# Optimization experiments

Measured on AMD Instinct MI355X. Metric: run time of the kernel, lower is better.

Reference implementation:

```python
import jax, jax.numpy as jnp
import numpy as np

N = 50000      # nodes
E = 800000     # edges (avg degree 16)
F_IN = 128     # input features
HID = 64       # hidden per head
HEADS = 4      # heads per layer
G = 256        # graphs in batch
C = 10         # classes
ALPHA = 0.01   # leaky relu negative slope


def setup_inputs() -> dict:
    key = jax.random.key(0)
    ks = jax.random.split(key, 12)
    x = jax.random.normal(ks[0], (N, F_IN), dtype=jnp.float32)
    edge_index = jax.random.randint(ks[1], (2, E), 0, N, dtype=jnp.int32)
    batch = jnp.sort(jax.random.randint(ks[2], (N,), 0, G, dtype=jnp.int32))

    def glorot(k, shape):
        fan_in = shape[0] if len(shape) == 2 else int(np.prod(shape[1:]))
        return (jax.random.normal(k, shape, dtype=jnp.float32) / np.float32(np.sqrt(fan_in)))

    W1 = glorot(ks[3], (F_IN, HEADS * HID))
    a1_src = glorot(ks[4], (HEADS, HID))
    a1_dst = glorot(ks[5], (HEADS, HID))
    W2 = glorot(ks[6], (HEADS * HID, HEADS * HID))
    a2_src = glorot(ks[7], (HEADS, HID))
    a2_dst = glorot(ks[8], (HEADS, HID))
    lin_W = glorot(ks[9], (2 * HEADS * HID, C))
    lin_b = jnp.zeros((C,), dtype=jnp.float32)
    return {
        "x": x, "edge_index": edge_index, "batch": batch,
        "W1": W1, "a1_src": a1_src, "a1_dst": a1_dst,
        "W2": W2, "a2_src": a2_src, "a2_dst": a2_dst,
        "lin_W": lin_W, "lin_b": lin_b,
    }


def _gat_layer(x, src, dst, W, a_src, a_dst):
    """Multi-head GAT layer: edge softmax over incoming neighbors, concat heads, ELU."""
    n = x.shape[0]
    h, f = a_src.shape
    Wh = (x @ W).reshape(n, h, f)                       # [N,H,F]
    # per-node attention logits (decomposed GAT attention a^T [Wh_i || Wh_j])
    ls = jnp.einsum("nhf,hf->nh", Wh, a_src)            # [N,H]
    ld = jnp.einsum("nhf,hf->nh", Wh, a_dst)            # [N,H]
    e = jax.nn.leaky_relu(ls[src] + ld[dst], ALPHA)      # [E,H]
    # numerically-stable softmax over edges grouped by destination node
    m = jax.ops.segment_max(e, dst, num_segments=n)      # [N,H]
    m = jnp.where(jnp.isfinite(m), m, 0.0)
    p = jnp.exp(e - m[dst])                              # [E,H]
    z = jax.ops.segment_sum(p, dst, num_segments=n)      # [N,H]
    attn = p / (z[dst] + 1e-16)                          # [E,H]
    msg = Wh[src] * attn[:, :, None]                     # [E,H,F]
    out = jax.ops.segment_sum(msg, dst, num_segments=n)  # [N,H,F]
    return jax.nn.elu(out.reshape(n, h * f))


def reference(x, edge_index, batch, W1, a1_src, a1_dst, W2, a2_src, a2_dst, lin_W, lin_b):
    src, dst = edge_index[0], edge_index[1]
    x = _gat_layer(x, src, dst, W1, a1_src, a1_dst)
    x = _gat_layer(x, src, dst, W2, a2_src, a2_dst)
    # global max / mean pool per graph
    mx = jax.ops.segment_max(x, batch, num_segments=G)
    mx = jnp.where(jnp.isfinite(mx), mx, 0.0)
    s = jax.ops.segment_sum(x, batch, num_segments=G)
    cnt = jax.ops.segment_sum(jnp.ones((x.shape[0], 1), x.dtype), batch, num_segments=G)
    mean = s / jnp.maximum(cnt, 1.0)
    pooled = jnp.concatenate([mx, mean], axis=1)         # [G, 2*H*F]
    return pooled @ lin_W + lin_b                        # [G, C]
```

## Files before the change

kernel.cpp:

```cpp
#include <hip/hip_runtime.h>
#include <hip/hip_bf16.h>

#define NNODES 50000
#define NEDGES 800000
#define FIN    128
#define HID    64
#define HEADS  4
#define NGRAPH 256
#define NCLS   10
#define DTOT   256
#define ALPHA  0.01f
#define CAPLG  6
#define CAP    (1 << CAPLG)

typedef short bf16x8 __attribute__((ext_vector_type(8)));
typedef float f32x4  __attribute__((ext_vector_type(4)));

#define NB      ((NNODES + 255) / 256)
#define EB      ((NEDGES + 255) / 256)
#define XB      ((NNODES * FIN / 4 + 255) / 256)
#define W1B     (FIN * DTOT / 256)
#define W2B     (DTOT * DTOT / 256)

__device__ __forceinline__ ushort f2bf(float v) {
    return __bfloat16_as_ushort(__float2bfloat16(v));
}
__device__ __forceinline__ float blo(unsigned u) { return __uint_as_float(u << 16); }
__device__ __forceinline__ float bhi(unsigned u) { return __uint_as_float(u & 0xffff0000u); }

__global__ __launch_bounds__(256) void k_setup(const int* __restrict__ src, const int* __restrict__ dst,
                                               int* __restrict__ cursor, int* __restrict__ esrc,
                                               const int* __restrict__ batch, int* __restrict__ gstart,
                                               const float4* __restrict__ x4, ushort4* __restrict__ xbf4,
                                               const float* __restrict__ W1, ushort* __restrict__ W1t,
                                               const float* __restrict__ W2, ushort* __restrict__ W2t) {
    int b = blockIdx.x, t = threadIdx.x;
    if (b < EB) {
        int e = b * 256 + t;
        if (e < NEDGES) {
            int d = dst[e];
            int pos = atomicAdd(&cursor[d], 1);
            if (pos < CAP) esrc[(d << CAPLG) + pos] = src[e];
        }
    } else if (b < EB + NB) {
        int i = (b - EB) * 256 + t;
        if (i >= NNODES) return;
        int bb = batch[i];
        if (i == 0) {
            for (int g = 0; g <= bb; ++g) gstart[g] = 0;
        } else {
            int pb = batch[i - 1];
            if (pb != bb) for (int g = pb + 1; g <= bb; ++g) gstart[g] = i;
        }
        if (i == NNODES - 1)
            for (int g = bb + 1; g <= NGRAPH; ++g) gstart[g] = NNODES;
    } else if (b < EB + NB + XB) {
        int i = (b - EB - NB) * 256 + t;
        if (i >= NNODES * FIN / 4) return;
        float4 v = x4[i];
        ushort4 o;
        o.x = f2bf(v.x); o.y = f2bf(v.y); o.z = f2bf(v.z); o.w = f2bf(v.w);
        xbf4[i] = o;
    } else if (b < EB + NB + XB + W1B) {
        int id = (b - EB - NB - XB) * 256 + t;
        int n = id & 255, k = id >> 8;
        W1t[n * FIN + (((k >> 3) ^ (n & 7)) << 3) + (k & 7)] = f2bf(W1[k * DTOT + n]);
    } else {
        int id = (b - EB - NB - XB - W1B) * 256 + t;
        int n = id & 255, k = id >> 8;
        W2t[n * DTOT + (((k >> 3) ^ (n & 7)) << 3) + (k & 7)] = f2bf(W2[k * DTOT + n]);
    }
}

template <int K>
__global__ __launch_bounds__(256) void k_gemm_mfma(const ushort* __restrict__ Abf,
                                                   const ushort* __restrict__ Bt,
                                                   ushort* __restrict__ Cbf,
                                                   float* __restrict__ ls,
                                                   float* __restrict__ ld_,
                                                   const float* __restrict__ a_src,
                                                   const float* __restrict__ a_dst,
                                                   int M) {
    __shared__ ushort Bl[128 * K];
    const int tid  = threadIdx.x;
    const int w    = tid >> 6;
    const int lane = tid & 63;
    const int l15  = lane & 15;
    const int quad = lane >> 4;
    const int m0 = blockIdx.y * 128;
    const int n0 = blockIdx.x * 128;
    const int hb = blockIdx.x * 2;

    {
        const uint4* sp = (const uint4*)(Bt + (size_t)n0 * K);
        uint4* dp = (uint4*)Bl;
#pragma unroll
        for (int idx = tid; idx < 128 * K / 8; idx += 256) dp[idx] = sp[idx];
    }
    __syncthreads();

    f32x4 acc[2][8];
#pragma unroll
    for (int mf = 0; mf < 2; ++mf)
#pragma unroll
        for (int nf = 0; nf < 8; ++nf)
            acc[mf][nf] = (f32x4){0.f, 0.f, 0.f, 0.f};

    const int rbase = m0 + w * 32;
    int rowA0 = rbase + l15;       if (rowA0 >= M) rowA0 = M - 1;
    int rowA1 = rbase + 16 + l15;  if (rowA1 >= M) rowA1 = M - 1;
    const ushort* pa0 = Abf + (size_t)rowA0 * K + quad * 8;
    const ushort* pa1 = Abf + (size_t)rowA1 * K + quad * 8;

#pragma unroll
    for (int ks = 0; ks < K / 32; ++ks) {
        bf16x8 a0 = *(const bf16x8*)(pa0 + ks * 32);
        bf16x8 a1 = *(const bf16x8*)(pa1 + ks * 32);
        bf16x8 bfr[8];
#pragma unroll
        for (int nf = 0; nf < 8; ++nf) {
            int n = nf * 16 + l15;
            int c = (ks * 4 + quad) ^ (n & 7);
            bfr[nf] = *(const bf16x8*)&Bl[n * K + (c << 3)];
        }
#pragma unroll
        for (int nf = 0; nf < 8; ++nf) {
            acc[0][nf] = __builtin_amdgcn_mfma_f32_16x16x32_bf16(a0, bfr[nf], acc[0][nf], 0, 0, 0);
            acc[1][nf] = __builtin_amdgcn_mfma_f32_16x16x32_bf16(a1, bfr[nf], acc[1][nf], 0, 0, 0);
        }
    }

    float as[8], ad[8];
#pragma unroll
    for (int nf = 0; nf < 8; ++nf) {
        int head = hb + (nf >> 2);
        as[nf] = a_src[head * HID + (nf & 3) * 16 + l15];
        ad[nf] = a_dst[head * HID + (nf & 3) * 16 + l15];
    }
#pragma unroll
    for (int mf = 0; mf < 2; ++mf) {
#pragma unroll
        for (int reg = 0; reg < 4; ++reg) {
            int row = rbase + mf * 16 + quad * 4 + reg;
            bool ok = row < M;
            if (ok) {
#pragma unroll
                for (int nf = 0; nf < 8; ++nf)
                    Cbf[(size_t)row * DTOT + n0 + nf * 16 + l15] = f2bf(acc[mf][nf][reg]);
            }
            float s0 = 0.f, d0 = 0.f, s1 = 0.f, d1 = 0.f;
#pragma unroll
            for (int nf = 0; nf < 4; ++nf) {
                s0 += acc[mf][nf][reg] * as[nf];
                d0 += acc[mf][nf][reg] * ad[nf];
                s1 += acc[mf][nf + 4][reg] * as[nf + 4];
                d1 += acc[mf][nf + 4][reg] * ad[nf + 4];
            }
#pragma unroll
            for (int off = 1; off < 16; off <<= 1) {
                s0 += __shfl_xor(s0, off);
                d0 += __shfl_xor(d0, off);
                s1 += __shfl_xor(s1, off);
                d1 += __shfl_xor(d1, off);
            }
            if (ok && l15 == 0) {
                ls[row * HEADS + hb]      = s0;
                ld_[row * HEADS + hb]     = d0;
                ls[row * HEADS + hb + 1]  = s1;
                ld_[row * HEADS + hb + 1] = d1;
            }
        }
    }
}

__global__ __launch_bounds__(256) void k_gat_aggr(const int* __restrict__ cnt,
                                                  const int* __restrict__ esrc,
                                                  const ushort* __restrict__ Whbf,
                                                  const float* __restrict__ ls,
                                                  const float* __restrict__ ld_,
                                                  ushort* __restrict__ out) {
    const int wv   = threadIdx.x >> 6;
    const int lane = threadIdx.x & 63;
    const int i    = blockIdx.x * 4 + wv;
    if (i >= NNODES) return;
    const int half = lane >> 5;
    const int l32  = lane & 31;
    const int h    = l32 >> 3;
    const int e0 = i << CAPLG;
    int deg = cnt[i]; if (deg > CAP) deg = CAP;
    const int e1 = e0 + deg;
    const float ldv = ld_[i * HEADS + h];

    float mx = -INFINITY;
    for (int e = e0 + (l32 & 7) + 8 * half; e < e1; e += 16)
        mx = fmaxf(mx, ls[esrc[e] * HEADS + h]);
    mx = fmaxf(mx, __shfl_xor(mx, 1));
    mx = fmaxf(mx, __shfl_xor(mx, 2));
    mx = fmaxf(mx, __shfl_xor(mx, 4));
    mx = fmaxf(mx, __shfl_xor(mx, 32));
    float lvm = mx + ldv;
    const float M = lvm > 0.f ? lvm : ALPHA * lvm;

    float ac[8] = {};
    float z = 0.f;
    const int ch = 8 * l32;
    int e = e0 + half;
    for (; e + 6 < e1; e += 8) {
        int s0 = esrc[e], s1 = esrc[e + 2], s2 = esrc[e + 4], s3 = esrc[e + 6];
        float l0 = ls[s0 * HEADS + h] + ldv;
        float l1 = ls[s1 * HEADS + h] + ldv;
        float l2 = ls[s2 * HEADS + h] + ldv;
        float l3 = ls[s3 * HEADS + h] + ldv;
        uint4 u0 = *(const uint4*)&Whbf[(size_t)s0 * DTOT + ch];
        uint4 u1 = *(const uint4*)&Whbf[(size_t)s1 * DTOT + ch];
        uint4 u2 = *(const uint4*)&Whbf[(size_t)s2 * DTOT + ch];
        uint4 u3 = *(const uint4*)&Whbf[(size_t)s3 * DTOT + ch];
        float p0 = __expf((l0 > 0.f ? l0 : ALPHA * l0) - M);
        float p1 = __expf((l1 > 0.f ? l1 : ALPHA * l1) - M);
        float p2 = __expf((l2 > 0.f ? l2 : ALPHA * l2) - M);
        float p3 = __expf((l3 > 0.f ? l3 : ALPHA * l3) - M);
        z += p0 + p1 + p2 + p3;
        ac[0] = fmaf(p0, blo(u0.x), ac[0]); ac[1] = fmaf(p0, bhi(u0.x), ac[1]);
        ac[2] = fmaf(p0, blo(u0.y), ac[2]); ac[3] = fmaf(p0, bhi(u0.y), ac[3]);
        ac[4] = fmaf(p0, blo(u0.z), ac[4]); ac[5] = fmaf(p0, bhi(u0.z), ac[5]);
        ac[6] = fmaf(p0, blo(u0.w), ac[6]); ac[7] = fmaf(p0, bhi(u0.w), ac[7]);
        ac[0] = fmaf(p1, blo(u1.x), ac[0]); ac[1] = fmaf(p1, bhi(u1.x), ac[1]);
        ac[2] = fmaf(p1, blo(u1.y), ac[2]); ac[3] = fmaf(p1, bhi(u1.y), ac[3]);
        ac[4] = fmaf(p1, blo(u1.z), ac[4]); ac[5] = fmaf(p1, bhi(u1.z), ac[5]);
        ac[6] = fmaf(p1, blo(u1.w), ac[6]); ac[7] = fmaf(p1, bhi(u1.w), ac[7]);
        ac[0] = fmaf(p2, blo(u2.x), ac[0]); ac[1] = fmaf(p2, bhi(u2.x), ac[1]);
        ac[2] = fmaf(p2, blo(u2.y), ac[2]); ac[3] = fmaf(p2, bhi(u2.y), ac[3]);
        ac[4] = fmaf(p2, blo(u2.z), ac[4]); ac[5] = fmaf(p2, bhi(u2.z), ac[5]);
        ac[6] = fmaf(p2, blo(u2.w), ac[6]); ac[7] = fmaf(p2, bhi(u2.w), ac[7]);
        ac[0] = fmaf(p3, blo(u3.x), ac[0]); ac[1] = fmaf(p3, bhi(u3.x), ac[1]);
        ac[2] = fmaf(p3, blo(u3.y), ac[2]); ac[3] = fmaf(p3, bhi(u3.y), ac[3]);
        ac[4] = fmaf(p3, blo(u3.z), ac[4]); ac[5] = fmaf(p3, bhi(u3.z), ac[5]);
        ac[6] = fmaf(p3, blo(u3.w), ac[6]); ac[7] = fmaf(p3, bhi(u3.w), ac[7]);
    }
    for (; e < e1; e += 2) {
        int s0 = esrc[e];
        float l0 = ls[s0 * HEADS + h] + ldv;
        uint4 u0 = *(const uint4*)&Whbf[(size_t)s0 * DTOT + ch];
        float p0 = __expf((l0 > 0.f ? l0 : ALPHA * l0) - M);
        z += p0;
        ac[0] = fmaf(p0, blo(u0.x), ac[0]); ac[1] = fmaf(p0, bhi(u0.x), ac[1]);
        ac[2] = fmaf(p0, blo(u0.y), ac[2]); ac[3] = fmaf(p0, bhi(u0.y), ac[3]);
        ac[4] = fmaf(p0, blo(u0.z), ac[4]); ac[5] = fmaf(p0, bhi(u0.z), ac[5]);
        ac[6] = fmaf(p0, blo(u0.w), ac[6]); ac[7] = fmaf(p0, bhi(u0.w), ac[7]);
    }

#pragma unroll
    for (int j = 0; j < 8; ++j) ac[j] += __shfl_xor(ac[j], 32);
    z += __shfl_xor(z, 32);

    if (half == 0) {
        const float inv = 1.f / (z + 1e-16f);
        float v[8];
#pragma unroll
        for (int j = 0; j < 8; ++j) {
            float t = ac[j] * inv;
            v[j] = t > 0.f ? t : __expf(t) - 1.f;
        }
        ushort4 pk, pk2;
        pk.x  = f2bf(v[0]); pk.y  = f2bf(v[1]); pk.z  = f2bf(v[2]); pk.w  = f2bf(v[3]);
        pk2.x = f2bf(v[4]); pk2.y = f2bf(v[5]); pk2.z = f2bf(v[6]); pk2.w = f2bf(v[7]);
        *(ushort4*)(out + (size_t)i * DTOT + ch)     = pk;
        *(ushort4*)(out + (size_t)i * DTOT + ch + 4) = pk2;
    }
}

__global__ __launch_bounds__(1024) void k_pool_final(const ushort* __restrict__ h2bf,
                                                     const int* __restrict__ gstart,
                                                     const float* __restrict__ W,
                                                     const float* __restrict__ b,
                                                     float* __restrict__ out) {
    __shared__ float smx[4][256];
    __shared__ float ssm[4][256];
    __shared__ float pooled[2 * DTOT];
    int g = blockIdx.x, t = threadIdx.x;
    int c = t & 255, j = t >> 8;
    int s = gstart[g], e = gstart[g + 1];
    float mx = -INFINITY, sm = 0.f;
    for (int n = s + j; n < e; n += 4) {
        float vv = __uint_as_float(((unsigned)h2bf[(size_t)n * DTOT + c]) << 16);
        mx = fmaxf(mx, vv);
        sm += vv;
    }
    smx[j][c] = mx;
    ssm[j][c] = sm;
    __syncthreads();
    if (t < 256) {
        float m = fmaxf(fmaxf(smx[0][t], smx[1][t]), fmaxf(smx[2][t], smx[3][t]));
        float su = ssm[0][t] + ssm[1][t] + ssm[2][t] + ssm[3][t];
        int cnt = e - s;
        if (cnt <= 0) m = 0.f;
        pooled[t] = m;
        pooled[DTOT + t] = su / (float)(cnt > 0 ? cnt : 1);
    }
    __syncthreads();
    int wv = t >> 6, lane = t & 63;
    if (wv < NCLS) {
        float acc = 0.f;
        for (int k = lane; k < 2 * DTOT; k += 64)
            acc += pooled[k] * W[k * NCLS + wv];
#pragma unroll
        for (int off = 32; off; off >>= 1) acc += __shfl_down(acc, off);
        if (lane == 0)
            out[g * NCLS + wv] = acc + b[wv];
    }
}

extern "C" void kernel_launch(void* const* d_in, const int* in_sizes, int n_in,
                              void* d_out, int out_size, void* d_ws, size_t ws_size,
                              hipStream_t stream) {
    const float* x     = (const float*)d_in[0];
    const int*   ei    = (const int*)d_in[1];
    const int*   batch = (const int*)d_in[2];
    const float* W1    = (const float*)d_in[3];
    const float* a1s   = (const float*)d_in[4];
    const float* a1d   = (const float*)d_in[5];
    const float* W2    = (const float*)d_in[6];
    const float* a2s   = (const float*)d_in[7];
    const float* a2d   = (const float*)d_in[8];
    const float* linW  = (const float*)d_in[9];
    const float* linb  = (const float*)d_in[10];
    float* out = (float*)d_out;

    const int* src = ei;
    const int* dst = ei + NEDGES;

    size_t off = 0;
    char* base = (char*)d_ws;
    auto alloc = [&](size_t bytes) -> void* {
        void* p = base + off;
        off += (bytes + 255) & ~(size_t)255;
        return p;
    };
    ushort* xbf    = (ushort*)alloc((size_t)NNODES * FIN * 2);
    ushort* Whbf   = (ushort*)alloc((size_t)NNODES * DTOT * 2);
    ushort* h1bf   = (ushort*)alloc((size_t)NNODES * DTOT * 2);
    ushort* h2bf   = (ushort*)alloc((size_t)NNODES * DTOT * 2);
    float*  ls     = (float*)alloc((size_t)NNODES * HEADS * 4);
    float*  ld_    = (float*)alloc((size_t)NNODES * HEADS * 4);
    int*    cursor = (int*)alloc((size_t)NNODES * 4);
    int*    esrc   = (int*)alloc((size_t)NNODES * CAP * 4);
    int*    gstart = (int*)alloc((size_t)(NGRAPH + 1) * 4);
    ushort* W1t    = (ushort*)alloc((size_t)DTOT * FIN * 2);
    ushort* W2t    = (ushort*)alloc((size_t)DTOT * DTOT * 2);

    hipMemsetAsync(cursor, 0, (size_t)NNODES * 4, stream);

    int setup_blocks = EB + NB + XB + W1B + W2B;
    k_setup<<<setup_blocks, 256, 0, stream>>>(src, dst, cursor, esrc, batch, gstart,
                                              (const float4*)x, (ushort4*)xbf,
                                              W1, W1t, W2, W2t);

    dim3 ggrid(2, (NNODES + 127) / 128);

    k_gemm_mfma<FIN><<<ggrid, 256, 0, stream>>>(xbf, W1t, Whbf, ls, ld_, a1s, a1d, NNODES);
    k_gat_aggr<<<(NNODES + 3) / 4, 256, 0, stream>>>(cursor, esrc, Whbf, ls, ld_, h1bf);

    k_gemm_mfma<DTOT><<<ggrid, 256, 0, stream>>>(h1bf, W2t, Whbf, ls, ld_, a2s, a2d, NNODES);
    k_gat_aggr<<<(NNODES + 3) / 4, 256, 0, stream>>>(cursor, esrc, Whbf, ls, ld_, h2bf);

    k_pool_final<<<NGRAPH, 1024, 0, stream>>>(h2bf, gstart, linW, linb, out);
}
```

Measured before the change: 325.5 us.

## Split GAT aggregation into attention pass and channel-sliced gather kernel

Replaces the fused per-node aggregation with two kernels. The first computes normalized edge attention per head and stores it as fp16 in a per-head binned array. The second gathers Wh rows in 32-channel slices, with slice-major block ordering so consecutive blocks reuse cache lines across nodes. Edge source indices are also narrowed to 16-bit to cut index traffic. The split adds an extra launch and attention-array traffic, and fp16 attention lowers precision. 16-bit indices only work because the node count fits in a ushort.

```diff
diff --git a/kernel.cpp b/kernel.cpp
--- a/kernel.cpp
+++ b/kernel.cpp
@@ -12,6 +12,9 @@
 #define ALPHA  0.01f
 #define CAPLG  6
 #define CAP    (1 << CAPLG)
+#define BINS   (NNODES << CAPLG)
+#define NGROUP 64
+#define GRPS   ((NNODES + NGROUP - 1) / NGROUP)
 
 typedef short bf16x8 __attribute__((ext_vector_type(8)));
 typedef float f32x4  __attribute__((ext_vector_type(4)));
@@ -29,7 +32,7 @@
 __device__ __forceinline__ float bhi(unsigned u) { return __uint_as_float(u & 0xffff0000u); }
 
 __global__ __launch_bounds__(256) void k_setup(const int* __restrict__ src, const int* __restrict__ dst,
-                                               int* __restrict__ cursor, int* __restrict__ esrc,
+                                               int* __restrict__ cursor, ushort* __restrict__ esrc,
                                                const int* __restrict__ batch, int* __restrict__ gstart,
                                                const float4* __restrict__ x4, ushort4* __restrict__ xbf4,
                                                const float* __restrict__ W1, ushort* __restrict__ W1t,
@@ -40,7 +43,7 @@
         if (e < NEDGES) {
             int d = dst[e];
             int pos = atomicAdd(&cursor[d], 1);
-            if (pos < CAP) esrc[(d << CAPLG) + pos] = src[e];
+            if (pos < CAP) esrc[(d << CAPLG) + pos] = (ushort)src[e];
         }
     } else if (b < EB + NB) {
         int i = (b - EB) * 256 + t;
@@ -173,99 +176,99 @@
     }
 }
 
-__global__ __launch_bounds__(256) void k_gat_aggr(const int* __restrict__ cnt,
-                                                  const int* __restrict__ esrc,
-                                                  const ushort* __restrict__ Whbf,
-                                                  const float* __restrict__ ls,
-                                                  const float* __restrict__ ld_,
-                                                  ushort* __restrict__ out) {
-    const int wv   = threadIdx.x >> 6;
-    const int lane = threadIdx.x & 63;
-    const int i    = blockIdx.x * 4 + wv;
+__global__ __launch_bounds__(256) void k_attn(const int* __restrict__ cnt,
+                                              const ushort* __restrict__ esrc,
+                                              const float* __restrict__ ls,
+                                              const float* __restrict__ ld_,
+                                              _Float16* __restrict__ attnp) {
+    int wv = threadIdx.x >> 6, lane = threadIdx.x & 63;
+    int i = blockIdx.x * 4 + wv;
     if (i >= NNODES) return;
-    const int half = lane >> 5;
-    const int l32  = lane & 31;
-    const int h    = l32 >> 3;
-    const int e0 = i << CAPLG;
+    int h = lane & 3, eo = lane >> 2;
     int deg = cnt[i]; if (deg > CAP) deg = CAP;
-    const int e1 = e0 + deg;
-    const float ldv = ld_[i * HEADS + h];
-
+    int e0 = i << CAPLG, e1 = e0 + deg;
+    float ldv = ld_[i * HEADS + h];
+    float lv[4];
     float mx = -INFINITY;
-    for (int e = e0 + (l32 & 7) + 8 * half; e < e1; e += 16)
-        mx = fmaxf(mx, ls[esrc[e] * HEADS + h]);
-    mx = fmaxf(mx, __shfl_xor(mx, 1));
-    mx = fmaxf(mx, __shfl_xor(mx, 2));
+#pragma unroll
+    for (int r = 0; r < 4; ++r) {
+        int e = e0 + eo + 16 * r;
+        float v = -INFINITY;
+        if (e < e1) {
+            float l = ls[(int)esrc[e] * HEADS + h] + ldv;
+            v = l > 0.f ? l : ALPHA * l;
+        }
+        lv[r] = v;
+        mx = fmaxf(mx, v);
+    }
     mx = fmaxf(mx, __shfl_xor(mx, 4));
+    mx = fmaxf(mx, __shfl_xor(mx, 8));
+    mx = fmaxf(mx, __shfl_xor(mx, 16));
     mx = fmaxf(mx, __shfl_xor(mx, 32));
-    float lvm = mx + ldv;
-    const float M = lvm > 0.f ? lvm : ALPHA * lvm;
-
-    float ac[8] = {};
+    float p[4];
     float z = 0.f;
-    const int ch = 8 * l32;
-    int e = e0 + half;
-    for (; e + 6 < e1; e += 8) {
-        int s0 = esrc[e], s1 = esrc[e + 2], s2 = esrc[e + 4], s3 = esrc[e + 6];
-        float l0 = ls[s0 * HEADS + h] + ldv;
-        float l1 = ls[s1 * HEADS + h] + ldv;
-        float l2 = ls[s2 * HEADS + h] + ldv;
-        float l3 = ls[s3 * HEADS + h] + ldv;
-        uint4 u0 = *(const uint4*)&Whbf[(size_t)s0 * DTOT + ch];
-        uint4 u1 = *(const uint4*)&Whbf[(size_t)s1 * DTOT + ch];
-        uint4 u2 = *(const uint4*)&Whbf[(size_t)s2 * DTOT + ch];
-        uint4 u3 = *(const uint4*)&Whbf[(size_t)s3 * DTOT + ch];
-        float p0 = __expf((l0 > 0.f ? l0 : ALPHA * l0) - M);
-        float p1 = __expf((l1 > 0.f ? l1 : ALPHA * l1) - M);
-        float p2 = __expf((l2 > 0.f ? l2 : ALPHA * l2) - M);
-        float p3 = __expf((l3 > 0.f ? l3 : ALPHA * l3) - M);
-        z += p0 + p1 + p2 + p3;
-        ac[0] = fmaf(p0, blo(u0.x), ac[0]); ac[1] = fmaf(p0, bhi(u0.x), ac[1]);
-        ac[2] = fmaf(p0, blo(u0.y), ac[2]); ac[3] = fmaf(p0, bhi(u0.y), ac[3]);
-        ac[4] = fmaf(p0, blo(u0.z), ac[4]); ac[5] = fmaf(p0, bhi(u0.z), ac[5]);
-        ac[6] = fmaf(p0, blo(u0.w), ac[6]); ac[7] = fmaf(p0, bhi(u0.w), ac[7]);
-        ac[0] = fmaf(p1, blo(u1.x), ac[0]); ac[1] = fmaf(p1, bhi(u1.x), ac[1]);
-        ac[2] = fmaf(p1, blo(u1.y), ac[2]); ac[3] = fmaf(p1, bhi(u1.y), ac[3]);
-        ac[4] = fmaf(p1, blo(u1.z), ac[4]); ac[5] = fmaf(p1, bhi(u1.z), ac[5]);
-        ac[6] = fmaf(p1, blo(u1.w), ac[6]); ac[7] = fmaf(p1, bhi(u1.w), ac[7]);
-        ac[0] = fmaf(p2, blo(u2.x), ac[0]); ac[1] = fmaf(p2, bhi(u2.x), ac[1]);
-        ac[2] = fmaf(p2, blo(u2.y), ac[2]); ac[3] = fmaf(p2, bhi(u2.y), ac[3]);
-        ac[4] = fmaf(p2, blo(u2.z), ac[4]); ac[5] = fmaf(p2, bhi(u2.z), ac[5]);
-        ac[6] = fmaf(p2, blo(u2.w), ac[6]); ac[7] = fmaf(p2, bhi(u2.w), ac[7]);
-        ac[0] = fmaf(p3, blo(u3.x), ac[0]); ac[1] = fmaf(p3, bhi(u3.x), ac[1]);
-        ac[2] = fmaf(p3, blo(u3.y), ac[2]); ac[3] = fmaf(p3, bhi(u3.y), ac[3]);
-        ac[4] = fmaf(p3, blo(u3.z), ac[4]); ac[5] = fmaf(p3, bhi(u3.z), ac[5]);
-        ac[6] = fmaf(p3, blo(u3.w), ac[6]); ac[7] = fmaf(p3, bhi(u3.w), ac[7]);
-    }
-    for (; e < e1; e += 2) {
-        int s0 = esrc[e];
-        float l0 = ls[s0 * HEADS + h] + ldv;
-        uint4 u0 = *(const uint4*)&Whbf[(size_t)s0 * DTOT + ch];
-        float p0 = __expf((l0 > 0.f ? l0 : ALPHA * l0) - M);
-        z += p0;
-        ac[0] = fmaf(p0, blo(u0.x), ac[0]); ac[1] = fmaf(p0, bhi(u0.x), ac[1]);
-        ac[2] = fmaf(p0, blo(u0.y), ac[2]); ac[3] = fmaf(p0, bhi(u0.y), ac[3]);
-        ac[4] = fmaf(p0, blo(u0.z), ac[4]); ac[5] = fmaf(p0, bhi(u0.z), ac[5]);
-        ac[6] = fmaf(p0, blo(u0.w), ac[6]); ac[7] = fmaf(p0, bhi(u0.w), ac[7]);
-    }
-
-#pragma unroll
-    for (int j = 0; j < 8; ++j) ac[j] += __shfl_xor(ac[j], 32);
+#pragma unroll
+    for (int r = 0; r < 4; ++r) {
+        p[r] = (lv[r] == -INFINITY) ? 0.f : __expf(lv[r] - mx);
+        z += p[r];
+    }
+    z += __shfl_xor(z, 4);
+    z += __shfl_xor(z, 8);
+    z += __shfl_xor(z, 16);
     z += __shfl_xor(z, 32);
-
-    if (half == 0) {
-        const float inv = 1.f / (z + 1e-16f);
-        float v[8];
-#pragma unroll
-        for (int j = 0; j < 8; ++j) {
-            float t = ac[j] * inv;
-            v[j] = t > 0.f ? t : __expf(t) - 1.f;
-        }
-        ushort4 pk, pk2;
-        pk.x  = f2bf(v[0]); pk.y  = f2bf(v[1]); pk.z  = f2bf(v[2]); pk.w  = f2bf(v[3]);
-        pk2.x = f2bf(v[4]); pk2.y = f2bf(v[5]); pk2.z = f2bf(v[6]); pk2.w = f2bf(v[7]);
-        *(ushort4*)(out + (size_t)i * DTOT + ch)     = pk;
-        *(ushort4*)(out + (size_t)i * DTOT + ch + 4) = pk2;
+    float inv = 1.f / (z + 1e-16f);
+#pragma unroll
+    for (int r = 0; r < 4; ++r) {
+        int e = e0 + eo + 16 * r;
+        if (e < e1) attnp[(size_t)h * BINS + e] = (_Float16)(p[r] * inv);
+    }
+}
+
+__global__ __launch_bounds__(256) void k_gat_slice(const int* __restrict__ cnt,
+                                                   const ushort* __restrict__ esrc,
+                                                   const ushort* __restrict__ Whbf,
+                                                   const _Float16* __restrict__ attnp,
+                                                   ushort* __restrict__ out) {
+    const int bx = blockIdx.x;
+    const int s  = bx & 7;
+    const int grp = bx >> 3;
+    const int wv = threadIdx.x >> 6, lane = threadIdx.x & 63;
+    const int eo = lane >> 4;
+    const int cl = lane & 15;
+    const int c0 = s * 32;
+    const _Float16* ap = attnp + (size_t)(s >> 1) * BINS;
+    const int nbase = grp * NGROUP + wv * (NGROUP / 4);
+#pragma unroll 1
+    for (int nn = 0; nn < NGROUP / 4; ++nn) {
+        int i = nbase + nn;
+        if (i >= NNODES) break;
+        int deg = cnt[i]; if (deg > CAP) deg = CAP;
+        int e0 = i << CAPLG, e1 = e0 + deg;
+        float a0 = 0.f, a1 = 0.f;
+        int e = e0 + eo;
+        for (; e + 4 < e1; e += 8) {
+            int s0 = (int)esrc[e], s1 = (int)esrc[e + 4];
+            float p0 = (float)ap[e];
+            float p1 = (float)ap[e + 4];
+            unsigned u0 = *(const unsigned*)&Whbf[(size_t)s0 * DTOT + c0 + 2 * cl];
+            unsigned u1 = *(const unsigned*)&Whbf[(size_t)s1 * DTOT + c0 + 2 * cl];
+            a0 = fmaf(p0, blo(u0), a0); a1 = fmaf(p0, bhi(u0), a1);
+            a0 = fmaf(p1, blo(u1), a0); a1 = fmaf(p1, bhi(u1), a1);
+        }
+        if (e < e1) {
+            int s0 = (int)esrc[e];
+            float p0 = (float)ap[e];
+            unsigned u0 = *(const unsigned*)&Whbf[(size_t)s0 * DTOT + c0 + 2 * cl];
+            a0 = fmaf(p0, blo(u0), a0); a1 = fmaf(p0, bhi(u0), a1);
+        }
+        a0 += __shfl_xor(a0, 16); a0 += __shfl_xor(a0, 32);
+        a1 += __shfl_xor(a1, 16); a1 += __shfl_xor(a1, 32);
+        if (eo == 0) {
+            float v0 = a0 > 0.f ? a0 : __expf(a0) - 1.f;
+            float v1 = a1 > 0.f ? a1 : __expf(a1) - 1.f;
+            unsigned pk = (unsigned)f2bf(v0) | ((unsigned)f2bf(v1) << 16);
+            *(unsigned*)&out[(size_t)i * DTOT + c0 + 2 * cl] = pk;
+        }
     }
 }
 
@@ -336,17 +339,18 @@
         off += (bytes + 255) & ~(size_t)255;
         return p;
     };
-    ushort* xbf    = (ushort*)alloc((size_t)NNODES * FIN * 2);
-    ushort* Whbf   = (ushort*)alloc((size_t)NNODES * DTOT * 2);
-    ushort* h1bf   = (ushort*)alloc((size_t)NNODES * DTOT * 2);
-    ushort* h2bf   = (ushort*)alloc((size_t)NNODES * DTOT * 2);
-    float*  ls     = (float*)alloc((size_t)NNODES * HEADS * 4);
-    float*  ld_    = (float*)alloc((size_t)NNODES * HEADS * 4);
-    int*    cursor = (int*)alloc((size_t)NNODES * 4);
-    int*    esrc   = (int*)alloc((size_t)NNODES * CAP * 4);
-    int*    gstart = (int*)alloc((size_t)(NGRAPH + 1) * 4);
-    ushort* W1t    = (ushort*)alloc((size_t)DTOT * FIN * 2);
-    ushort* W2t    = (ushort*)alloc((size_t)DTOT * DTOT * 2);
+    ushort*    xbf    = (ushort*)alloc((size_t)NNODES * FIN * 2);
+    ushort*    Whbf   = (ushort*)alloc((size_t)NNODES * DTOT * 2);
+    ushort*    h1bf   = (ushort*)alloc((size_t)NNODES * DTOT * 2);
+    ushort*    h2bf   = (ushort*)alloc((size_t)NNODES * DTOT * 2);
+    float*     ls     = (float*)alloc((size_t)NNODES * HEADS * 4);
+    float*     ld_    = (float*)alloc((size_t)NNODES * HEADS * 4);
+    int*       cursor = (int*)alloc((size_t)NNODES * 4);
+    ushort*    esrc   = (ushort*)alloc((size_t)BINS * 2);
+    _Float16*  attnp  = (_Float16*)alloc((size_t)HEADS * BINS * 2);
+    int*       gstart = (int*)alloc((size_t)(NGRAPH + 1) * 4);
+    ushort*    W1t    = (ushort*)alloc((size_t)DTOT * FIN * 2);
+    ushort*    W2t    = (ushort*)alloc((size_t)DTOT * DTOT * 2);
 
     hipMemsetAsync(cursor, 0, (size_t)NNODES * 4, stream);
 
@@ -356,12 +360,16 @@
                                               W1, W1t, W2, W2t);
 
     dim3 ggrid(2, (NNODES + 127) / 128);
+    int attn_blocks = (NNODES + 3) / 4;
+    int gat_blocks  = GRPS * 8;
 
     k_gemm_mfma<FIN><<<ggrid, 256, 0, stream>>>(xbf, W1t, Whbf, ls, ld_, a1s, a1d, NNODES);
-    k_gat_aggr<<<(NNODES + 3) / 4, 256, 0, stream>>>(cursor, esrc, Whbf, ls, ld_, h1bf);
+    k_attn<<<attn_blocks, 256, 0, stream>>>(cursor, esrc, ls, ld_, attnp);
+    k_gat_slice<<<gat_blocks, 256, 0, stream>>>(cursor, esrc, Whbf, attnp, h1bf);
 
     k_gemm_mfma<DTOT><<<ggrid, 256, 0, stream>>>(h1bf, W2t, Whbf, ls, ld_, a2s, a2d, NNODES);
-    k_gat_aggr<<<(NNODES + 3) / 4, 256, 0, stream>>>(cursor, esrc, Whbf, ls, ld_, h2bf);
+    k_attn<<<attn_blocks, 256, 0, stream>>>(cursor, esrc, ls, ld_, attnp);
+    k_gat_slice<<<gat_blocks, 256, 0, stream>>>(cursor, esrc, Whbf, attnp, h2bf);
 
     k_pool_final<<<NGRAPH, 1024, 0, stream>>>(h2bf, gstart, linW, linb, out);
 }
```

Result: slower. 530.0 us (+62.8%).
